# Kernel tuning notes

Hardware: AMD Instinct MI355X
Metric: run time of the kernel (lower is better)

Reference implementation:

```python
import jax, jax.numpy as jnp
import numpy as np

N_NODES = 50000
N_EDGES = 800000
D_IN = 64
F1 = 64
F2 = 64
D_HID = 100


def setup_inputs() -> dict:
    key = jax.random.key(0)
    ks = jax.random.split(key, 12)
    x = jax.random.normal(ks[0], (N_NODES, D_IN), dtype=jnp.float32)
    edge_src = jax.random.randint(ks[1], (N_EDGES,), 0, N_NODES, dtype=jnp.int32)
    edge_dst = jax.random.randint(ks[2], (N_EDGES,), 0, N_NODES, dtype=jnp.int32)
    # stands in for pre-normalized GCN adjacency values (D^-1/2 (A+I) D^-1/2)
    edge_weight = jax.random.uniform(ks[3], (N_EDGES,), dtype=jnp.float32)
    def glorot(k, shape):
        lim = np.sqrt(6.0 / (shape[0] + shape[1]))
        return jax.random.uniform(k, shape, jnp.float32, -lim, lim)
    W1 = glorot(ks[4], (D_IN, F1))
    b1 = jnp.zeros((F1,), jnp.float32)
    W2 = glorot(ks[5], (F1, F2))
    b2 = jnp.zeros((F2,), jnp.float32)
    Wd = glorot(ks[6], (F2, D_HID))
    bd = jnp.zeros((D_HID,), jnp.float32)
    Wo = glorot(ks[7], (D_HID, 1))
    bo = jnp.zeros((1,), jnp.float32)
    return {"x": x, "edge_src": edge_src, "edge_dst": edge_dst,
            "edge_weight": edge_weight, "W1": W1, "b1": b1, "W2": W2,
            "b2": b2, "Wd": Wd, "bd": bd, "Wo": Wo, "bo": bo}


def _gcn_conv(x, edge_src, edge_dst, edge_weight, W, b):
    # spektral GCNConv: out = swish(A_norm @ (X @ W) + b)
    h = x @ W                                        # [N, F]
    msg = h[edge_src] * edge_weight[:, None]          # [E, F] gather + scale
    agg = jax.ops.segment_sum(msg, edge_dst, num_segments=N_NODES)  # [N, F]
    return jax.nn.swish(agg + b)


def reference(x, edge_src, edge_dst, edge_weight, W1, b1, W2, b2, Wd, bd, Wo, bo):
    h = _gcn_conv(x, edge_src, edge_dst, edge_weight, W1, b1)
    h = _gcn_conv(h, edge_src, edge_dst, edge_weight, W2, b2)
    h = jax.nn.swish(h @ Wd + bd)                    # Dense(100, swish)
    return jax.nn.sigmoid(h @ Wo + bo)               # Dense(1, sigmoid) -> [N, 1]
```

## Files before the change

### kernel.cpp

```cpp
#include <hip/hip_runtime.h>

#define N_NODES 50000
#define N_EDGES 800000
#define D 64
#define DHID 100
#define NTILES (N_NODES / 16)
#define SCAN_BLOCKS ((N_NODES + 1023) / 1024)

typedef unsigned short ushort;
typedef unsigned int uint;
typedef __attribute__((ext_vector_type(8))) short s16x8;
typedef __attribute__((ext_vector_type(4))) float f32x4;

#define MFMA16(A, B, C) __builtin_amdgcn_mfma_f32_16x16x32_bf16((A), (B), (C), 0, 0, 0)

__device__ __forceinline__ float swishf(float x) { return x / (1.0f + __expf(-x)); }

__device__ __forceinline__ ushort f2bf(float f) {
    uint u = __float_as_uint(f);
    uint r = (u + 0x7fffu + ((u >> 16) & 1u)) >> 16;
    return (ushort)r;
}
__device__ __forceinline__ float bf2f(ushort h) { return __uint_as_float((uint)h << 16); }
__device__ __forceinline__ float bf_lo(uint d) { return __uint_as_float(d << 16); }
__device__ __forceinline__ float bf_hi(uint d) { return __uint_as_float(d & 0xffff0000u); }

__device__ __forceinline__ void accum8(float* acc, uint4 v, float w) {
    acc[0] = fmaf(w, bf_lo(v.x), acc[0]);
    acc[1] = fmaf(w, bf_hi(v.x), acc[1]);
    acc[2] = fmaf(w, bf_lo(v.y), acc[2]);
    acc[3] = fmaf(w, bf_hi(v.y), acc[3]);
    acc[4] = fmaf(w, bf_lo(v.z), acc[4]);
    acc[5] = fmaf(w, bf_hi(v.z), acc[5]);
    acc[6] = fmaf(w, bf_lo(v.w), acc[6]);
    acc[7] = fmaf(w, bf_hi(v.w), acc[7]);
}

__global__ __launch_bounds__(256) void hist_rank(const int* __restrict__ dst,
                                                 int* __restrict__ deg,
                                                 int* __restrict__ rank) {
    int e = blockIdx.x * 256 + threadIdx.x;
    if (e < N_EDGES) rank[e] = atomicAdd(&deg[dst[e]], 1);
}

__global__ __launch_bounds__(1024) void scanA(const int* __restrict__ deg,
                                              int* __restrict__ partial,
                                              int* __restrict__ blockSums) {
    __shared__ int tile[1024];
    int i = blockIdx.x * 1024 + threadIdx.x;
    int v = (i < N_NODES) ? deg[i] : 0;
    tile[threadIdx.x] = v;
    __syncthreads();
    for (int off = 1; off < 1024; off <<= 1) {
        int t = (threadIdx.x >= (unsigned)off) ? tile[threadIdx.x - off] : 0;
        __syncthreads();
        tile[threadIdx.x] += t;
        __syncthreads();
    }
    if (i < N_NODES) partial[i] = tile[threadIdx.x] - v;
    if (threadIdx.x == 1023) blockSums[blockIdx.x] = tile[1023];
}

__global__ __launch_bounds__(64) void scanB(int* __restrict__ blockSums,
                                            int* __restrict__ partial) {
    int lane = threadIdx.x;
    int v = (lane < SCAN_BLOCKS) ? blockSums[lane] : 0;
    int incl = v;
#pragma unroll
    for (int off = 1; off < 64; off <<= 1) {
        int t = __shfl_up(incl, off, 64);
        if (lane >= off) incl += t;
    }
    if (lane < SCAN_BLOCKS) blockSums[lane] = incl - v;
    if (lane == SCAN_BLOCKS - 1) partial[N_NODES] = v;
}

__global__ __launch_bounds__(256) void fill_kernel(const int* __restrict__ src,
                                                   const int* __restrict__ dst,
                                                   const float* __restrict__ w,
                                                   const int* __restrict__ rank,
                                                   const int* __restrict__ partial,
                                                   const int* __restrict__ blockSums,
                                                   float2* __restrict__ csr) {
    int e = blockIdx.x * 256 + threadIdx.x;
    if (e < N_EDGES) {
        int d = dst[e];
        int p = partial[d] + blockSums[d >> 10] + rank[e];
        csr[p] = make_float2(__int_as_float(src[e]), w[e]);
    }
}

__global__ __launch_bounds__(256) void mfma_l1(const float* __restrict__ X,
                                               const float* __restrict__ W,
                                               ushort* __restrict__ H) {
    __shared__ __align__(16) short sBT[2][D][72];
    __shared__ __align__(16) short rep[4][16][72];
    int tid = threadIdx.x;
    for (int idx = tid; idx < D * D; idx += 256) {
        int k = idx >> 6, c = idx & 63;
        float wv = W[idx];
        ushort hi = f2bf(wv);
        ushort lo = f2bf(wv - bf2f(hi));
        sBT[0][c][k] = (short)hi;
        sBT[1][c][k] = (short)lo;
    }
    __syncthreads();
    int w = tid >> 6, lane = tid & 63, quad = lane >> 4, m = lane & 15;
    int tile = blockIdx.x * 4 + w;
    if (tile >= NTILES) return;
    int node0 = tile * 16;

    f32x4 acc[4] = {{0,0,0,0},{0,0,0,0},{0,0,0,0},{0,0,0,0}};
#pragma unroll
    for (int kt = 0; kt < 2; ++kt) {
        int k0 = kt * 32 + quad * 8;
        const float* xp = X + ((size_t)(node0 + m) << 6) + k0;
        float4 xa = *((const float4*)xp);
        float4 xb = *((const float4*)(xp + 4));
        float xv[8] = {xa.x, xa.y, xa.z, xa.w, xb.x, xb.y, xb.z, xb.w};
        s16x8 ahi, alo;
#pragma unroll
        for (int j = 0; j < 8; ++j) {
            ushort hi = f2bf(xv[j]);
            ahi[j] = (short)hi;
            alo[j] = (short)f2bf(xv[j] - bf2f(hi));
        }
#pragma unroll
        for (int ct = 0; ct < 4; ++ct) {
            int n = ct * 16 + m;
            s16x8 bhi = *((const s16x8*)&sBT[0][n][k0]);
            s16x8 blo = *((const s16x8*)&sBT[1][n][k0]);
            acc[ct] = MFMA16(ahi, bhi, acc[ct]);
            acc[ct] = MFMA16(ahi, blo, acc[ct]);
            acc[ct] = MFMA16(alo, bhi, acc[ct]);
        }
    }
#pragma unroll
    for (int ct = 0; ct < 4; ++ct)
#pragma unroll
        for (int r = 0; r < 4; ++r)
            rep[w][quad * 4 + r][ct * 16 + m] = (short)f2bf(acc[ct][r]);
#pragma unroll
    for (int half = 0; half < 2; ++half) {
        int r = (lane >> 3) + half * 8;
        int c0 = (lane & 7) * 8;
        s16x8 v = *((const s16x8*)&rep[w][r][c0]);
        *((s16x8*)(H + ((size_t)(node0 + r) << 6) + c0)) = v;
    }
}

__global__ __launch_bounds__(256) void mfma_l2(const ushort* __restrict__ act,
                                               const float* __restrict__ W,
                                               ushort* __restrict__ H) {
    __shared__ __align__(16) short sBT[2][D][72];
    __shared__ __align__(16) short rep[4][16][72];
    int tid = threadIdx.x;
    for (int idx = tid; idx < D * D; idx += 256) {
        int k = idx >> 6, c = idx & 63;
        float wv = W[idx];
        ushort hi = f2bf(wv);
        ushort lo = f2bf(wv - bf2f(hi));
        sBT[0][c][k] = (short)hi;
        sBT[1][c][k] = (short)lo;
    }
    __syncthreads();
    int w = tid >> 6, lane = tid & 63, quad = lane >> 4, m = lane & 15;
    int tile = blockIdx.x * 4 + w;
    if (tile >= NTILES) return;
    int node0 = tile * 16;

    f32x4 acc[4] = {{0,0,0,0},{0,0,0,0},{0,0,0,0},{0,0,0,0}};
#pragma unroll
    for (int kt = 0; kt < 2; ++kt) {
        int k0 = kt * 32 + quad * 8;
        s16x8 a = *((const s16x8*)(act + ((size_t)(node0 + m) << 6) + k0));
#pragma unroll
        for (int ct = 0; ct < 4; ++ct) {
            int n = ct * 16 + m;
            s16x8 bhi = *((const s16x8*)&sBT[0][n][k0]);
            s16x8 blo = *((const s16x8*)&sBT[1][n][k0]);
            acc[ct] = MFMA16(a, bhi, acc[ct]);
            acc[ct] = MFMA16(a, blo, acc[ct]);
        }
    }
#pragma unroll
    for (int ct = 0; ct < 4; ++ct)
#pragma unroll
        for (int r = 0; r < 4; ++r)
            rep[w][quad * 4 + r][ct * 16 + m] = (short)f2bf(acc[ct][r]);
#pragma unroll
    for (int half = 0; half < 2; ++half) {
        int r = (lane >> 3) + half * 8;
        int c0 = (lane & 7) * 8;
        s16x8 v = *((const s16x8*)&rep[w][r][c0]);
        *((s16x8*)(H + ((size_t)(node0 + r) << 6) + c0)) = v;
    }
}

__global__ __launch_bounds__(256) void gather_act(const ushort* __restrict__ H,
                                                  const int* __restrict__ partial,
                                                  const int* __restrict__ blockSums,
                                                  const float2* __restrict__ csr,
                                                  const float* __restrict__ bias,
                                                  ushort* __restrict__ actOut) {
    int tid = threadIdx.x;
    int wave = tid >> 6, lane = tid & 63;
    int j = lane >> 3, fg = lane & 7;
    int node = blockIdx.x * 4 + wave;
    int beg = partial[node] + blockSums[node >> 10];
    int np1 = node + 1;
    int end = partial[np1] + blockSums[np1 >> 10];

    float acc[8] = {0, 0, 0, 0, 0, 0, 0, 0};
    int last = end - 1;
    for (int base = beg; base < end; base += 32) {
        int i0 = base + j, i1 = i0 + 8, i2 = i0 + 16, i3 = i0 + 24;
        float2 e0 = csr[min(i0, last)];
        float2 e1 = csr[min(i1, last)];
        float2 e2 = csr[min(i2, last)];
        float2 e3 = csr[min(i3, last)];
        float w0 = (i0 < end) ? e0.y : 0.f;
        float w1 = (i1 < end) ? e1.y : 0.f;
        float w2 = (i2 < end) ? e2.y : 0.f;
        float w3 = (i3 < end) ? e3.y : 0.f;
        uint4 v0 = *((const uint4*)(H + ((size_t)__float_as_int(e0.x) << 6) + (fg << 3)));
        uint4 v1 = *((const uint4*)(H + ((size_t)__float_as_int(e1.x) << 6) + (fg << 3)));
        uint4 v2 = *((const uint4*)(H + ((size_t)__float_as_int(e2.x) << 6) + (fg << 3)));
        uint4 v3 = *((const uint4*)(H + ((size_t)__float_as_int(e3.x) << 6) + (fg << 3)));
        accum8(acc, v0, w0);
        accum8(acc, v1, w1);
        accum8(acc, v2, w2);
        accum8(acc, v3, w3);
    }
#pragma unroll
    for (int t = 0; t < 8; ++t) {
        acc[t] += __shfl_xor(acc[t], 8, 64);
        acc[t] += __shfl_xor(acc[t], 16, 64);
        acc[t] += __shfl_xor(acc[t], 32, 64);
    }
    if (j == 0) {
        float4 ba = ((const float4*)bias)[fg * 2];
        float4 bb = ((const float4*)bias)[fg * 2 + 1];
        float r0 = swishf(acc[0] + ba.x);
        float r1 = swishf(acc[1] + ba.y);
        float r2 = swishf(acc[2] + ba.z);
        float r3 = swishf(acc[3] + ba.w);
        float r4 = swishf(acc[4] + bb.x);
        float r5 = swishf(acc[5] + bb.y);
        float r6 = swishf(acc[6] + bb.z);
        float r7 = swishf(acc[7] + bb.w);
        uint4 u;
        u.x = (uint)f2bf(r0) | ((uint)f2bf(r1) << 16);
        u.y = (uint)f2bf(r2) | ((uint)f2bf(r3) << 16);
        u.z = (uint)f2bf(r4) | ((uint)f2bf(r5) << 16);
        u.w = (uint)f2bf(r6) | ((uint)f2bf(r7) << 16);
        *((uint4*)(actOut + ((size_t)node << 6) + (fg << 3))) = u;
    }
}

#define NCT 7
__global__ __launch_bounds__(256) void mfma_head(const ushort* __restrict__ act2,
                                                 const float* __restrict__ Wd,
                                                 const float* __restrict__ bd,
                                                 const float* __restrict__ Wo,
                                                 const float* __restrict__ bo,
                                                 float* __restrict__ out) {
    __shared__ __align__(16) short sBT[2][NCT * 16][72];
    __shared__ float sbd[NCT * 16];
    __shared__ float sWo[NCT * 16];
    int tid = threadIdx.x;
    for (int idx = tid; idx < NCT * 16 * D; idx += 256) {
        int jj = idx >> 6, k = idx & 63;
        float wv = (jj < DHID) ? Wd[k * DHID + jj] : 0.f;
        ushort hi = f2bf(wv);
        ushort lo = f2bf(wv - bf2f(hi));
        sBT[0][jj][k] = (short)hi;
        sBT[1][jj][k] = (short)lo;
    }
    if (tid < NCT * 16) {
        sbd[tid] = (tid < DHID) ? bd[tid] : 0.f;
        sWo[tid] = (tid < DHID) ? Wo[tid] : 0.f;
    }
    __syncthreads();
    int w = tid >> 6, lane = tid & 63, quad = lane >> 4, m = lane & 15;
    int tile = blockIdx.x * 4 + w;
    if (tile >= NTILES) return;
    int node0 = tile * 16;

    f32x4 acc[NCT];
#pragma unroll
    for (int ct = 0; ct < NCT; ++ct) acc[ct] = (f32x4){0, 0, 0, 0};
#pragma unroll
    for (int kt = 0; kt < 2; ++kt) {
        int k0 = kt * 32 + quad * 8;
        s16x8 a = *((const s16x8*)(act2 + ((size_t)(node0 + m) << 6) + k0));
#pragma unroll
        for (int ct = 0; ct < NCT; ++ct) {
            int n = ct * 16 + m;
            s16x8 bhi = *((const s16x8*)&sBT[0][n][k0]);
            s16x8 blo = *((const s16x8*)&sBT[1][n][k0]);
            acc[ct] = MFMA16(a, bhi, acc[ct]);
            acc[ct] = MFMA16(a, blo, acc[ct]);
        }
    }
    float part[4] = {0, 0, 0, 0};
#pragma unroll
    for (int ct = 0; ct < NCT; ++ct) {
        int jj = ct * 16 + m;
        float bdv = sbd[jj], wov = sWo[jj];
#pragma unroll
        for (int r = 0; r < 4; ++r)
            part[r] = fmaf(swishf(acc[ct][r] + bdv), wov, part[r]);
    }
#pragma unroll
    for (int r = 0; r < 4; ++r) {
        part[r] += __shfl_xor(part[r], 1, 64);
        part[r] += __shfl_xor(part[r], 2, 64);
        part[r] += __shfl_xor(part[r], 4, 64);
        part[r] += __shfl_xor(part[r], 8, 64);
    }
    if (m == 0) {
        float b0 = bo[0];
        float4 o;
        o.x = 1.f / (1.f + __expf(-(part[0] + b0)));
        o.y = 1.f / (1.f + __expf(-(part[1] + b0)));
        o.z = 1.f / (1.f + __expf(-(part[2] + b0)));
        o.w = 1.f / (1.f + __expf(-(part[3] + b0)));
        *((float4*)(out + node0 + quad * 4)) = o;
    }
}

extern "C" void kernel_launch(void* const* d_in, const int* in_sizes, int n_in,
                              void* d_out, int out_size, void* d_ws, size_t ws_size,
                              hipStream_t stream) {
    const float* x   = (const float*)d_in[0];
    const int* esrc  = (const int*)d_in[1];
    const int* edst  = (const int*)d_in[2];
    const float* ew  = (const float*)d_in[3];
    const float* W1  = (const float*)d_in[4];
    const float* b1  = (const float*)d_in[5];
    const float* W2  = (const float*)d_in[6];
    const float* b2  = (const float*)d_in[7];
    const float* Wd  = (const float*)d_in[8];
    const float* bd  = (const float*)d_in[9];
    const float* Wo  = (const float*)d_in[10];
    const float* bo  = (const float*)d_in[11];
    float* out = (float*)d_out;

    char* ws = (char*)d_ws;
    ushort* H1   = (ushort*)ws;  ws += (size_t)N_NODES * D * sizeof(ushort);
    ushort* act1 = (ushort*)ws;  ws += (size_t)N_NODES * D * sizeof(ushort);
    ushort* H2   = (ushort*)ws;  ws += (size_t)N_NODES * D * sizeof(ushort);
    ushort* act2 = (ushort*)ws;  ws += (size_t)N_NODES * D * sizeof(ushort);
    float2* csr  = (float2*)ws;  ws += (size_t)N_EDGES * sizeof(float2);
    int* rank    = (int*)ws;     ws += (size_t)N_EDGES * sizeof(int);
    int* partial = (int*)ws;     ws += (size_t)(N_NODES + 16) * sizeof(int);
    int* deg     = (int*)ws;     ws += (size_t)N_NODES * sizeof(int);
    int* blockSums = (int*)ws;

    const int edgeBlocks = (N_EDGES + 255) / 256;
    const int mmBlocks   = (NTILES + 3) / 4;
    const int gBlocks    = N_NODES / 4;

    hipMemsetAsync(deg, 0, N_NODES * sizeof(int), stream);
    hist_rank<<<edgeBlocks, 256, 0, stream>>>(edst, deg, rank);
    scanA<<<SCAN_BLOCKS, 1024, 0, stream>>>(deg, partial, blockSums);
    scanB<<<1, 64, 0, stream>>>(blockSums, partial);
    fill_kernel<<<edgeBlocks, 256, 0, stream>>>(esrc, edst, ew, rank, partial, blockSums, csr);

    mfma_l1<<<mmBlocks, 256, 0, stream>>>(x, W1, H1);
    gather_act<<<gBlocks, 256, 0, stream>>>(H1, partial, blockSums, csr, b1, act1);

    mfma_l2<<<mmBlocks, 256, 0, stream>>>(act1, W2, H2);
    gather_act<<<gBlocks, 256, 0, stream>>>(H2, partial, blockSums, csr, b2, act2);

    mfma_head<<<mmBlocks, 256, 0, stream>>>(act2, Wd, bd, Wo, bo, out);
}
```

Baseline: 220.1 us.

## Fuse gather-aggregate with following dense matmul and head into single kernels

Merges each gather/aggregation kernel with the next MFMA matmul (layer 2 weights, or the dense+output head). Each 1024-thread block gathers 16 nodes into shared memory, then runs the MFMA on them. This removes two launches and the global round-trips for act1/act2. In exchange, every block redoes the weight conversion into LDS (3125 blocks each converting W), and the large blocks with barriers may lower occupancy and gather latency hiding.

```diff
diff --git a/kernel.cpp b/kernel.cpp
--- a/kernel.cpp
+++ b/kernel.cpp
@@ -6,6 +6,7 @@
 #define DHID 100
 #define NTILES (N_NODES / 16)
 #define SCAN_BLOCKS ((N_NODES + 1023) / 1024)
+#define NCT 7
 
 typedef unsigned short ushort;
 typedef unsigned int uint;
@@ -149,69 +150,10 @@
     }
 }
 
-__global__ __launch_bounds__(256) void mfma_l2(const ushort* __restrict__ act,
-                                               const float* __restrict__ W,
-                                               ushort* __restrict__ H) {
-    __shared__ __align__(16) short sBT[2][D][72];
-    __shared__ __align__(16) short rep[4][16][72];
-    int tid = threadIdx.x;
-    for (int idx = tid; idx < D * D; idx += 256) {
-        int k = idx >> 6, c = idx & 63;
-        float wv = W[idx];
-        ushort hi = f2bf(wv);
-        ushort lo = f2bf(wv - bf2f(hi));
-        sBT[0][c][k] = (short)hi;
-        sBT[1][c][k] = (short)lo;
-    }
-    __syncthreads();
-    int w = tid >> 6, lane = tid & 63, quad = lane >> 4, m = lane & 15;
-    int tile = blockIdx.x * 4 + w;
-    if (tile >= NTILES) return;
-    int node0 = tile * 16;
-
-    f32x4 acc[4] = {{0,0,0,0},{0,0,0,0},{0,0,0,0},{0,0,0,0}};
-#pragma unroll
-    for (int kt = 0; kt < 2; ++kt) {
-        int k0 = kt * 32 + quad * 8;
-        s16x8 a = *((const s16x8*)(act + ((size_t)(node0 + m) << 6) + k0));
-#pragma unroll
-        for (int ct = 0; ct < 4; ++ct) {
-            int n = ct * 16 + m;
-            s16x8 bhi = *((const s16x8*)&sBT[0][n][k0]);
-            s16x8 blo = *((const s16x8*)&sBT[1][n][k0]);
-            acc[ct] = MFMA16(a, bhi, acc[ct]);
-            acc[ct] = MFMA16(a, blo, acc[ct]);
-        }
-    }
-#pragma unroll
-    for (int ct = 0; ct < 4; ++ct)
-#pragma unroll
-        for (int r = 0; r < 4; ++r)
-            rep[w][quad * 4 + r][ct * 16 + m] = (short)f2bf(acc[ct][r]);
-#pragma unroll
-    for (int half = 0; half < 2; ++half) {
-        int r = (lane >> 3) + half * 8;
-        int c0 = (lane & 7) * 8;
-        s16x8 v = *((const s16x8*)&rep[w][r][c0]);
-        *((s16x8*)(H + ((size_t)(node0 + r) << 6) + c0)) = v;
-    }
-}
-
-__global__ __launch_bounds__(256) void gather_act(const ushort* __restrict__ H,
-                                                  const int* __restrict__ partial,
-                                                  const int* __restrict__ blockSums,
-                                                  const float2* __restrict__ csr,
-                                                  const float* __restrict__ bias,
-                                                  ushort* __restrict__ actOut) {
-    int tid = threadIdx.x;
-    int wave = tid >> 6, lane = tid & 63;
-    int j = lane >> 3, fg = lane & 7;
-    int node = blockIdx.x * 4 + wave;
-    int beg = partial[node] + blockSums[node >> 10];
-    int np1 = node + 1;
-    int end = partial[np1] + blockSums[np1 >> 10];
-
-    float acc[8] = {0, 0, 0, 0, 0, 0, 0, 0};
+__device__ __forceinline__ void gather_wave(const ushort* __restrict__ H,
+                                            const float2* __restrict__ csr,
+                                            int beg, int end, int j, int fg,
+                                            float* acc) {
     int last = end - 1;
     for (int base = beg; base < end; base += 32) {
         int i0 = base + j, i1 = i0 + 8, i2 = i0 + 16, i3 = i0 + 24;
@@ -238,38 +180,102 @@
         acc[t] += __shfl_xor(acc[t], 16, 64);
         acc[t] += __shfl_xor(acc[t], 32, 64);
     }
+}
+
+__global__ __launch_bounds__(1024) void gather_mm(const ushort* __restrict__ H,
+                                                  const int* __restrict__ partial,
+                                                  const int* __restrict__ blockSums,
+                                                  const float2* __restrict__ csr,
+                                                  const float* __restrict__ bias,
+                                                  const float* __restrict__ W,
+                                                  ushort* __restrict__ Hout) {
+    __shared__ __align__(16) short sBT[2][D][72];
+    __shared__ __align__(16) short sAct[16][72];
+    __shared__ __align__(16) short rep[4][16][20];
+    int tid = threadIdx.x;
+    for (int idx = tid; idx < D * D; idx += 1024) {
+        int k = idx >> 6, c = idx & 63;
+        float wv = W[idx];
+        ushort hi = f2bf(wv);
+        ushort lo = f2bf(wv - bf2f(hi));
+        sBT[0][c][k] = (short)hi;
+        sBT[1][c][k] = (short)lo;
+    }
+
+    int w = tid >> 6, lane = tid & 63;
+    int j = lane >> 3, fg = lane & 7;
+    int node0 = blockIdx.x * 16;
+    int node = node0 + w;
+    int beg = partial[node] + blockSums[node >> 10];
+    int np1 = node + 1;
+    int end = partial[np1] + blockSums[np1 >> 10];
+
+    float acc[8] = {0, 0, 0, 0, 0, 0, 0, 0};
+    gather_wave(H, csr, beg, end, j, fg, acc);
     if (j == 0) {
         float4 ba = ((const float4*)bias)[fg * 2];
         float4 bb = ((const float4*)bias)[fg * 2 + 1];
-        float r0 = swishf(acc[0] + ba.x);
-        float r1 = swishf(acc[1] + ba.y);
-        float r2 = swishf(acc[2] + ba.z);
-        float r3 = swishf(acc[3] + ba.w);
-        float r4 = swishf(acc[4] + bb.x);
-        float r5 = swishf(acc[5] + bb.y);
-        float r6 = swishf(acc[6] + bb.z);
-        float r7 = swishf(acc[7] + bb.w);
+        ushort r0 = f2bf(swishf(acc[0] + ba.x));
+        ushort r1 = f2bf(swishf(acc[1] + ba.y));
+        ushort r2 = f2bf(swishf(acc[2] + ba.z));
+        ushort r3 = f2bf(swishf(acc[3] + ba.w));
+        ushort r4 = f2bf(swishf(acc[4] + bb.x));
+        ushort r5 = f2bf(swishf(acc[5] + bb.y));
+        ushort r6 = f2bf(swishf(acc[6] + bb.z));
+        ushort r7 = f2bf(swishf(acc[7] + bb.w));
         uint4 u;
-        u.x = (uint)f2bf(r0) | ((uint)f2bf(r1) << 16);
-        u.y = (uint)f2bf(r2) | ((uint)f2bf(r3) << 16);
-        u.z = (uint)f2bf(r4) | ((uint)f2bf(r5) << 16);
-        u.w = (uint)f2bf(r6) | ((uint)f2bf(r7) << 16);
-        *((uint4*)(actOut + ((size_t)node << 6) + (fg << 3))) = u;
-    }
-}
-
-#define NCT 7
-__global__ __launch_bounds__(256) void mfma_head(const ushort* __restrict__ act2,
-                                                 const float* __restrict__ Wd,
-                                                 const float* __restrict__ bd,
-                                                 const float* __restrict__ Wo,
-                                                 const float* __restrict__ bo,
-                                                 float* __restrict__ out) {
+        u.x = (uint)r0 | ((uint)r1 << 16);
+        u.y = (uint)r2 | ((uint)r3 << 16);
+        u.z = (uint)r4 | ((uint)r5 << 16);
+        u.w = (uint)r6 | ((uint)r7 << 16);
+        *((uint4*)&sAct[w][fg * 8]) = u;
+    }
+    __syncthreads();
+
+    if (w < 4) {
+        int quad = lane >> 4, m = lane & 15;
+        f32x4 c4 = {0, 0, 0, 0};
+#pragma unroll
+        for (int kt = 0; kt < 2; ++kt) {
+            int k0 = kt * 32 + quad * 8;
+            s16x8 a = *((const s16x8*)&sAct[m][k0]);
+            s16x8 bhi = *((const s16x8*)&sBT[0][w * 16 + m][k0]);
+            s16x8 blo = *((const s16x8*)&sBT[1][w * 16 + m][k0]);
+            c4 = MFMA16(a, bhi, c4);
+            c4 = MFMA16(a, blo, c4);
+        }
+#pragma unroll
+        for (int r = 0; r < 4; ++r)
+            rep[w][quad * 4 + r][m] = (short)f2bf(c4[r]);
+    }
+    __syncthreads();
+
+    if (tid < 256) {
+        int r = tid >> 4;
+        int cg = tid & 15;
+        int col = cg * 4;
+        uint2 v = *((const uint2*)&rep[col >> 4][r][col & 15]);
+        *((uint2*)(Hout + ((size_t)(node0 + r) << 6) + col)) = v;
+    }
+}
+
+__global__ __launch_bounds__(1024) void gather_head(const ushort* __restrict__ H,
+                                                    const int* __restrict__ partial,
+                                                    const int* __restrict__ blockSums,
+                                                    const float2* __restrict__ csr,
+                                                    const float* __restrict__ bias,
+                                                    const float* __restrict__ Wd,
+                                                    const float* __restrict__ bd,
+                                                    const float* __restrict__ Wo,
+                                                    const float* __restrict__ bo,
+                                                    float* __restrict__ out) {
     __shared__ __align__(16) short sBT[2][NCT * 16][72];
+    __shared__ __align__(16) short sAct[16][72];
     __shared__ float sbd[NCT * 16];
     __shared__ float sWo[NCT * 16];
+    __shared__ float redBuf[NCT][17];
     int tid = threadIdx.x;
-    for (int idx = tid; idx < NCT * 16 * D; idx += 256) {
+    for (int idx = tid; idx < NCT * 16 * D; idx += 1024) {
         int jj = idx >> 6, k = idx & 63;
         float wv = (jj < DHID) ? Wd[k * DHID + jj] : 0.f;
         ushort hi = f2bf(wv);
@@ -281,52 +287,75 @@
         sbd[tid] = (tid < DHID) ? bd[tid] : 0.f;
         sWo[tid] = (tid < DHID) ? Wo[tid] : 0.f;
     }
-    __syncthreads();
-    int w = tid >> 6, lane = tid & 63, quad = lane >> 4, m = lane & 15;
-    int tile = blockIdx.x * 4 + w;
-    if (tile >= NTILES) return;
-    int node0 = tile * 16;
-
-    f32x4 acc[NCT];
-#pragma unroll
-    for (int ct = 0; ct < NCT; ++ct) acc[ct] = (f32x4){0, 0, 0, 0};
-#pragma unroll
-    for (int kt = 0; kt < 2; ++kt) {
-        int k0 = kt * 32 + quad * 8;
-        s16x8 a = *((const s16x8*)(act2 + ((size_t)(node0 + m) << 6) + k0));
-#pragma unroll
-        for (int ct = 0; ct < NCT; ++ct) {
-            int n = ct * 16 + m;
-            s16x8 bhi = *((const s16x8*)&sBT[0][n][k0]);
-            s16x8 blo = *((const s16x8*)&sBT[1][n][k0]);
-            acc[ct] = MFMA16(a, bhi, acc[ct]);
-            acc[ct] = MFMA16(a, blo, acc[ct]);
-        }
-    }
-    float part[4] = {0, 0, 0, 0};
-#pragma unroll
-    for (int ct = 0; ct < NCT; ++ct) {
-        int jj = ct * 16 + m;
+
+    int w = tid >> 6, lane = tid & 63;
+    int j = lane >> 3, fg = lane & 7;
+    int node0 = blockIdx.x * 16;
+    int node = node0 + w;
+    int beg = partial[node] + blockSums[node >> 10];
+    int np1 = node + 1;
+    int end = partial[np1] + blockSums[np1 >> 10];
+
+    float acc[8] = {0, 0, 0, 0, 0, 0, 0, 0};
+    gather_wave(H, csr, beg, end, j, fg, acc);
+    if (j == 0) {
+        float4 ba = ((const float4*)bias)[fg * 2];
+        float4 bb = ((const float4*)bias)[fg * 2 + 1];
+        ushort r0 = f2bf(swishf(acc[0] + ba.x));
+        ushort r1 = f2bf(swishf(acc[1] + ba.y));
+        ushort r2 = f2bf(swishf(acc[2] + ba.z));
+        ushort r3 = f2bf(swishf(acc[3] + ba.w));
+        ushort r4 = f2bf(swishf(acc[4] + bb.x));
+        ushort r5 = f2bf(swishf(acc[5] + bb.y));
+        ushort r6 = f2bf(swishf(acc[6] + bb.z));
+        ushort r7 = f2bf(swishf(acc[7] + bb.w));
+        uint4 u;
+        u.x = (uint)r0 | ((uint)r1 << 16);
+        u.y = (uint)r2 | ((uint)r3 << 16);
+        u.z = (uint)r4 | ((uint)r5 << 16);
+        u.w = (uint)r6 | ((uint)r7 << 16);
+        *((uint4*)&sAct[w][fg * 8]) = u;
+    }
+    __syncthreads();
+
+    if (w < NCT) {
+        int quad = lane >> 4, m = lane & 15;
+        f32x4 c4 = {0, 0, 0, 0};
+#pragma unroll
+        for (int kt = 0; kt < 2; ++kt) {
+            int k0 = kt * 32 + quad * 8;
+            s16x8 a = *((const s16x8*)&sAct[m][k0]);
+            s16x8 bhi = *((const s16x8*)&sBT[0][w * 16 + m][k0]);
+            s16x8 blo = *((const s16x8*)&sBT[1][w * 16 + m][k0]);
+            c4 = MFMA16(a, bhi, c4);
+            c4 = MFMA16(a, blo, c4);
+        }
+        int jj = w * 16 + m;
         float bdv = sbd[jj], wov = sWo[jj];
+        float part[4];
 #pragma unroll
         for (int r = 0; r < 4; ++r)
-            part[r] = fmaf(swishf(acc[ct][r] + bdv), wov, part[r]);
-    }
-#pragma unroll
-    for (int r = 0; r < 4; ++r) {
-        part[r] += __shfl_xor(part[r], 1, 64);
-        part[r] += __shfl_xor(part[r], 2, 64);
-        part[r] += __shfl_xor(part[r], 4, 64);
-        part[r] += __shfl_xor(part[r], 8, 64);
-    }
-    if (m == 0) {
-        float b0 = bo[0];
-        float4 o;
-        o.x = 1.f / (1.f + __expf(-(part[0] + b0)));
-        o.y = 1.f / (1.f + __expf(-(part[1] + b0)));
-        o.z = 1.f / (1.f + __expf(-(part[2] + b0)));
-        o.w = 1.f / (1.f + __expf(-(part[3] + b0)));
-        *((float4*)(out + node0 + quad * 4)) = o;
+            part[r] = swishf(c4[r] + bdv) * wov;
+#pragma unroll
+        for (int r = 0; r < 4; ++r) {
+            part[r] += __shfl_xor(part[r], 1, 64);
+            part[r] += __shfl_xor(part[r], 2, 64);
+            part[r] += __shfl_xor(part[r], 4, 64);
+            part[r] += __shfl_xor(part[r], 8, 64);
+        }
+        if (m == 0) {
+#pragma unroll
+            for (int r = 0; r < 4; ++r)
+                redBuf[w][quad * 4 + r] = part[r];
+        }
+    }
+    __syncthreads();
+
+    if (tid < 16) {
+        float z = bo[0];
+#pragma unroll
+        for (int t = 0; t < NCT; ++t) z += redBuf[t][tid];
+        out[node0 + tid] = 1.f / (1.f + __expf(-z));
     }
 }
 
@@ -349,9 +378,7 @@
 
     char* ws = (char*)d_ws;
     ushort* H1   = (ushort*)ws;  ws += (size_t)N_NODES * D * sizeof(ushort);
-    ushort* act1 = (ushort*)ws;  ws += (size_t)N_NODES * D * sizeof(ushort);
     ushort* H2   = (ushort*)ws;  ws += (size_t)N_NODES * D * sizeof(ushort);
-    ushort* act2 = (ushort*)ws;  ws += (size_t)N_NODES * D * sizeof(ushort);
     float2* csr  = (float2*)ws;  ws += (size_t)N_EDGES * sizeof(float2);
     int* rank    = (int*)ws;     ws += (size_t)N_EDGES * sizeof(int);
     int* partial = (int*)ws;     ws += (size_t)(N_NODES + 16) * sizeof(int);
@@ -360,7 +387,6 @@
 
     const int edgeBlocks = (N_EDGES + 255) / 256;
     const int mmBlocks   = (NTILES + 3) / 4;
-    const int gBlocks    = N_NODES / 4;
 
     hipMemsetAsync(deg, 0, N_NODES * sizeof(int), stream);
     hist_rank<<<edgeBlocks, 256, 0, stream>>>(edst, deg, rank);
@@ -369,10 +395,8 @@
     fill_kernel<<<edgeBlocks, 256, 0, stream>>>(esrc, edst, ew, rank, partial, blockSums, csr);
 
     mfma_l1<<<mmBlocks, 256, 0, stream>>>(x, W1, H1);
-    gather_act<<<gBlocks, 256, 0, stream>>>(H1, partial, blockSums, csr, b1, act1);
-
-    mfma_l2<<<mmBlocks, 256, 0, stream>>>(act1, W2, H2);
-    gather_act<<<gBlocks, 256, 0, stream>>>(H2, partial, blockSums, csr, b2, act2);
-
-    mfma_head<<<mmBlocks, 256, 0, stream>>>(act2, Wd, bd, Wo, bo, out);
-}
+
+    gather_mm<<<NTILES, 1024, 0, stream>>>(H1, partial, blockSums, csr, b1, W2, H2);
+
+    gather_head<<<NTILES, 1024, 0, stream>>>(H2, partial, blockSums, csr, b2, Wd, bd, Wo, bo, out);
+}
```

Measured after the change: 234.5 us. +6.5%, slower.
